# Kernel optimization log

Hardware: AMD Instinct MI355X
Metric: run time of the kernel (lower is better)

The kernel has to match this reference:

```python
import jax, jax.numpy as jnp
import numpy as np

H = 16       # num_heads (groups for complex conv)
A = 32       # num frequency anchors
KSZ = 5      # complex conv kernel size
PAD = (KSZ - 1) // 2  # circular padding, matches ComplexConv1DLayer


def setup_inputs() -> dict:
    key = jax.random.key(0)
    ks = jax.random.split(key, 12)
    B, N, D = 4, 2048, 1024
    hid, ghid = 256, 256  # pooling MLP hidden, gate MLP hidden
    F = N // 2 + 1

    def rn(k, shp, s=0.02):
        return jax.random.normal(k, shp, jnp.float32) * s

    return {
        "x": jax.random.normal(ks[0], (B, N, D), jnp.float32),
        "Wv": rn(ks[1], (D, D)), "bv": jnp.zeros((D,), jnp.float32),
        "Wp1": rn(ks[2], (D, hid)), "bp1": jnp.zeros((hid,), jnp.float32),
        "Wp2": rn(ks[3], (hid, 1)), "bp2": jnp.zeros((1,), jnp.float32),
        "Wg1": rn(ks[4], (D, ghid)), "bg1": jnp.zeros((ghid,), jnp.float32),
        "Wg2": rn(ks[5], (ghid, 2 * H * A)), "bg2": jnp.zeros((2 * H * A,), jnp.float32),
        "mod_bias": jnp.zeros((F,), jnp.float32),
        "conv_kr": rn(ks[6], (KSZ,), 1.0 / np.sqrt(KSZ)),
        "conv_ki": rn(ks[7], (KSZ,), 1.0 / np.sqrt(KSZ)),
        "Wo": rn(ks[8], (D, D)), "bo": jnp.zeros((D,), jnp.float32),
    }


def reference(x, Wv, bv, Wp1, bp1, Wp2, bp2, Wg1, bg1, Wg2, bg2,
              mod_bias, conv_kr, conv_ki, Wo, bo):
    B, N, D = x.shape
    dh = D // H
    F = N // 2 + 1

    # value projection -> per-head sequences, rFFT over sequence axis
    v = (x @ Wv + bv).reshape(B, N, H, dh).transpose(0, 2, 1, 3)   # (B,H,N,dh)
    Vf = jnp.fft.rfft(v, axis=2)                                   # (B,H,F,dh) complex64

    # AttentionPoolingLayer: two-layer MLP scores -> softmax over seq -> weighted sum
    s = jax.nn.gelu(x @ Wp1 + bp1, approximate=False) @ Wp2 + bp2  # (B,N,1)
    w = jax.nn.softmax(s, axis=1)
    g = jnp.sum(x * w, axis=1)                                     # (B,D)

    # gate MLP -> complex anchors (B,H,A)
    a = (jax.nn.gelu(g @ Wg1 + bg1, approximate=False) @ Wg2 + bg2).reshape(B, H, A, 2)
    anch_r, anch_i = a[..., 0], a[..., 1]

    # ComplexInterpolationLayer: cubic interpolation of anchors to F bins
    gr = jax.image.resize(anch_r, (B, H, F), method="cubic")
    gi = jax.image.resize(anch_i, (B, H, F), method="cubic")
    gate = gr + 1j * gi                                            # (B,H,F)

    # ComplexModReLULayer: ReLU(|z|+b) * z / |z| with per-frequency bias
    mag = jnp.abs(gate)
    gate = gate * (jax.nn.relu(mag + mod_bias) / (mag + 1e-8))

    # ComplexConv1DLayer: circular-pad complex conv along frequency
    gp = jnp.concatenate([gate[..., -PAD:], gate, gate[..., :PAD]], axis=-1)
    ker = conv_kr.astype(jnp.complex64) + 1j * conv_ki.astype(jnp.complex64)
    gate = sum(ker[j] * gp[..., j:j + F] for j in range(KSZ))      # (B,H,F)

    # spectral gating + inverse FFT + output projection
    y = jnp.fft.irfft(Vf * gate[..., None], n=N, axis=2)           # (B,H,N,dh)
    y = y.transpose(0, 2, 1, 3).reshape(B, N, D)
    return y @ Wo + bo
```

## Files before the change

### kernel.cpp

```cpp
#include <hip/hip_runtime.h>
#include <math.h>

#define NSEQ 2048
#define DMOD 1024
#define NBATCH 4
#define NHEAD 16
#define NFREQ 1025

typedef unsigned short u16t;
typedef __attribute__((ext_vector_type(8))) short short8;
typedef __attribute__((ext_vector_type(4))) float f32x4;

__device__ __forceinline__ float gelu_exact(float x) {
  return 0.5f * x * (1.0f + erff(x * 0.70710678118654752440f));
}
__device__ __forceinline__ u16t bf16_rtn(float x) {
  unsigned u = __float_as_uint(x);
  return (u16t)((u + 0x7FFFu + ((u >> 16) & 1u)) >> 16);
}
__device__ __forceinline__ float bf16f(u16t h) {
  return __uint_as_float(((unsigned)h) << 16);
}
__device__ __forceinline__ void gload_lds16(const u16t* g, u16t* l) {
  __builtin_amdgcn_global_load_lds(
      (const __attribute__((address_space(1))) void*)g,
      (__attribute__((address_space(3))) void*)l, 16, 0, 0);
}

__global__ __launch_bounds__(256) void split_kernel(const float* __restrict__ in,
    u16t* __restrict__ hi, u16t* __restrict__ lo, int n8) {
  for (int i = blockIdx.x * blockDim.x + threadIdx.x; i < n8; i += gridDim.x * blockDim.x) {
    const float4* p = reinterpret_cast<const float4*>(in + (size_t)i * 8);
    float4 a = p[0], b = p[1];
    float vv[8] = {a.x, a.y, a.z, a.w, b.x, b.y, b.z, b.w};
    alignas(16) u16t th[8];
    alignas(16) u16t tl[8];
#pragma unroll
    for (int e = 0; e < 8; ++e) {
      u16t h = bf16_rtn(vv[e]);
      th[e] = h;
      tl[e] = bf16_rtn(vv[e] - bf16f(h));
    }
    *reinterpret_cast<uint4*>(hi + (size_t)i * 8) = *reinterpret_cast<const uint4*>(th);
    *reinterpret_cast<uint4*>(lo + (size_t)i * 8) = *reinterpret_cast<const uint4*>(tl);
  }
}

__global__ __launch_bounds__(256) void tsplit_kernel(const float* __restrict__ W,
    u16t* __restrict__ Th, u16t* __restrict__ Tl, int K, int N) {
  __shared__ float tile[32][33];
  int k0 = blockIdx.y * 32, n0 = blockIdx.x * 32;
  int r = threadIdx.x >> 5, c = threadIdx.x & 31;
#pragma unroll
  for (int i = 0; i < 4; ++i)
    tile[r + 8 * i][c] = W[(size_t)(k0 + r + 8 * i) * N + n0 + c];
  __syncthreads();
#pragma unroll
  for (int i = 0; i < 4; ++i) {
    int rr = r + 8 * i;
    float v = tile[c][rr];
    u16t h = bf16_rtn(v);
    Th[(size_t)(n0 + rr) * K + k0 + c] = h;
    Tl[(size_t)(n0 + rr) * K + k0 + c] = bf16_rtn(v - bf16f(h));
  }
}

#define GEMM_KLOOP(Ah_g, Al_g, Bh_g, Bl_g, K, m0, n0)                                  \
  for (int k0 = 0; k0 < (K); k0 += 64) {                                               \
    _Pragma("unroll")                                                                  \
    for (int q = 0; q < 4; ++q) {                                                      \
      int cid = q * 256 + tid;                                                         \
      int row = cid >> 3, grp = cid & 7;                                               \
      int koff = k0 + ((grp ^ (row & 7)) << 3);                                        \
      size_t ea = (size_t)((m0) + row) * (K) + koff;                                   \
      size_t eb = (size_t)((n0) + row) * (K) + koff;                                   \
      int lbase = q * 2048 + wave * 512;                                               \
      gload_lds16((Ah_g) + ea, Ahs + lbase);                                           \
      gload_lds16((Al_g) + ea, Als + lbase);                                           \
      gload_lds16((Bh_g) + eb, Bhs + lbase);                                           \
      gload_lds16((Bl_g) + eb, Bls + lbase);                                           \
    }                                                                                  \
    __syncthreads();                                                                   \
    _Pragma("unroll")                                                                  \
    for (int kf = 0; kf < 2; ++kf) {                                                   \
      short8 ah[4], al[4];                                                             \
      _Pragma("unroll")                                                                \
      for (int mi = 0; mi < 4; ++mi) {                                                 \
        int r_ = wm0 + mi * 16 + lr;                                                   \
        int g = (kf * 4 + lg) ^ (r_ & 7);                                              \
        ah[mi] = *reinterpret_cast<const short8*>(&Ahs[r_ * 64 + g * 8]);              \
        al[mi] = *reinterpret_cast<const short8*>(&Als[r_ * 64 + g * 8]);              \
      }                                                                                \
      _Pragma("unroll")                                                                \
      for (int ni = 0; ni < 4; ++ni) {                                                 \
        int r_ = wn0 + ni * 16 + lr;                                                   \
        int g = (kf * 4 + lg) ^ (r_ & 7);                                              \
        short8 bh8 = *reinterpret_cast<const short8*>(&Bhs[r_ * 64 + g * 8]);          \
        short8 bl8 = *reinterpret_cast<const short8*>(&Bls[r_ * 64 + g * 8]);          \
        _Pragma("unroll")                                                              \
        for (int mi = 0; mi < 4; ++mi) {                                               \
          acc[mi][ni] = __builtin_amdgcn_mfma_f32_16x16x32_bf16(ah[mi], bh8, acc[mi][ni], 0, 0, 0); \
          acc[mi][ni] = __builtin_amdgcn_mfma_f32_16x16x32_bf16(ah[mi], bl8, acc[mi][ni], 0, 0, 0); \
          acc[mi][ni] = __builtin_amdgcn_mfma_f32_16x16x32_bf16(al[mi], bh8, acc[mi][ni], 0, 0, 0); \
        }                                                                              \
      }                                                                                \
    }                                                                                  \
    __syncthreads();                                                                   \
  }

__global__ __launch_bounds__(256) void gemm_fused_kernel(
    const u16t* __restrict__ Ah_g, const u16t* __restrict__ Al_g,
    const u16t* __restrict__ Bvh, const u16t* __restrict__ Bvl,
    const u16t* __restrict__ Bph, const u16t* __restrict__ Bpl,
    const float* __restrict__ bv, const float* __restrict__ bp1,
    const float* __restrict__ Wp2,
    float* __restrict__ vT, float* __restrict__ s_part) {
  __shared__ u16t Ahs[128 * 64], Als[128 * 64], Bhs[128 * 64], Bls[128 * 64];
  const int tid = threadIdx.x;
  const int lane = tid & 63, wave = tid >> 6;
  const int lr = lane & 15, lg = lane >> 4;
  const int wm0 = (wave >> 1) * 64, wn0 = (wave & 1) * 64;
  const int nwg = gridDim.x;
  const int L = (blockIdx.x & 7) * (nwg >> 3) + (blockIdx.x >> 3);
  const int m0 = (L / 10) * 128;
  const int nblk = L % 10;
  const bool vpath = (nblk < 8);
  const int n0 = vpath ? nblk * 128 : (nblk - 8) * 128;
  const u16t* Bh_g = vpath ? Bvh : Bph;
  const u16t* Bl_g = vpath ? Bvl : Bpl;
  const int K = 1024;

  f32x4 acc[4][4];
#pragma unroll
  for (int i = 0; i < 4; ++i)
#pragma unroll
    for (int j = 0; j < 4; ++j) acc[i][j] = 0.0f;

  GEMM_KLOOP(Ah_g, Al_g, Bh_g, Bl_g, K, m0, n0)

  if (vpath) {
#pragma unroll
    for (int mi = 0; mi < 4; ++mi)
#pragma unroll
      for (int ni = 0; ni < 4; ++ni) {
        int col = n0 + wn0 + ni * 16 + lr;
        float bvv = bv[col];
        f32x4 a = acc[mi][ni];
        int mbase = m0 + wm0 + mi * 16 + lg * 4;
        int b = mbase >> 11, ss = mbase & 2047;
        float4 o4;
        o4.x = a[0] + bvv; o4.y = a[1] + bvv; o4.z = a[2] + bvv; o4.w = a[3] + bvv;
        *reinterpret_cast<float4*>(vT + (size_t)b * (DMOD * NSEQ) + (size_t)col * NSEQ + ss) = o4;
      }
  } else {
    float w2[4], bcol[4];
#pragma unroll
    for (int ni = 0; ni < 4; ++ni) {
      int col = n0 + wn0 + ni * 16 + lr;
      w2[ni] = Wp2[col];
      bcol[ni] = bp1[col];
    }
    int chunk = (nblk - 8) * 2 + (wave & 1);
#pragma unroll
    for (int mi = 0; mi < 4; ++mi)
#pragma unroll
      for (int r = 0; r < 4; ++r) {
        float p = 0.f;
#pragma unroll
        for (int ni = 0; ni < 4; ++ni)
          p = fmaf(gelu_exact(acc[mi][ni][r] + bcol[ni]), w2[ni], p);
        p += __shfl_xor(p, 1);
        p += __shfl_xor(p, 2);
        p += __shfl_xor(p, 4);
        p += __shfl_xor(p, 8);
        if (lr == 0) {
          int row = m0 + wm0 + mi * 16 + lg * 4 + r;
          s_part[chunk * 8192 + row] = p;
        }
      }
  }
}

template<int NBLK>
__global__ __launch_bounds__(256) void mfma_gemm(
    const u16t* __restrict__ Ah_g, const u16t* __restrict__ Al_g,
    const u16t* __restrict__ Bh_g, const u16t* __restrict__ Bl_g,
    const float* __restrict__ bias,
    float* __restrict__ Cf,
    int N, int K) {
  __shared__ u16t Ahs[128 * 64], Als[128 * 64], Bhs[128 * 64], Bls[128 * 64];
  const int tid = threadIdx.x;
  const int lane = tid & 63, wave = tid >> 6;
  const int lr = lane & 15, lg = lane >> 4;
  const int wm0 = (wave >> 1) * 64, wn0 = (wave & 1) * 64;
  const int nwg = gridDim.x;
  const int L = (blockIdx.x & 7) * (nwg >> 3) + (blockIdx.x >> 3);
  const int m0 = (L / NBLK) * 128, n0 = (L % NBLK) * 128;

  f32x4 acc[4][4];
#pragma unroll
  for (int i = 0; i < 4; ++i)
#pragma unroll
    for (int j = 0; j < 4; ++j) acc[i][j] = 0.0f;

  GEMM_KLOOP(Ah_g, Al_g, Bh_g, Bl_g, K, m0, n0)

#pragma unroll
  for (int mi = 0; mi < 4; ++mi)
#pragma unroll
    for (int ni = 0; ni < 4; ++ni) {
      int col = n0 + wn0 + ni * 16 + lr;
      float bvv = bias[col];
      f32x4 a = acc[mi][ni];
#pragma unroll
      for (int r = 0; r < 4; ++r) {
        int row = m0 + wm0 + mi * 16 + lg * 4 + r;
        Cf[(size_t)row * N + col] = a[r] + bvv;
      }
    }
}

#define PADI(i) ((i) + ((i) >> 5))

template<int HJ, int TWS>
__device__ __forceinline__ void fwd_reg_stage(float* vr, float* vi,
    const float* TWr, const float* TWi, int lane) {
  float twr_[HJ], twi_[HJ];
#pragma unroll
  for (int t = 0; t < HJ; ++t) {
    int m = (t * 64 + lane) * TWS;
    twr_[t] = TWr[PADI(m)]; twi_[t] = TWi[PADI(m)];
  }
#pragma unroll
  for (int j = 0; j < 16; ++j) {
    if (j & HJ) continue;
    int t = j & (HJ - 1);
    float ur = vr[j], ui = vi[j];
    float wr = vr[j + HJ], wi = vi[j + HJ];
    float dr = ur - wr, di = ui - wi;
    vr[j] = ur + wr; vi[j] = ui + wi;
    vr[j + HJ] = dr * twr_[t] - di * twi_[t];
    vi[j + HJ] = dr * twi_[t] + di * twr_[t];
  }
}

template<int S, int TWS>
__device__ __forceinline__ void fwd_lane_stage(float* vr, float* vi,
    const float* TWr, const float* TWi, int lane) {
  float twr_ = 1.0f, twi_ = 0.0f;
  if (S > 1) {
    int m = (lane & (S - 1)) * TWS;
    twr_ = TWr[PADI(m)]; twi_ = TWi[PADI(m)];
  }
  bool hi = (lane & S) != 0;
#pragma unroll
  for (int j = 0; j < 16; ++j) {
    float or_ = __shfl_xor(vr[j], S, 64);
    float oi_ = __shfl_xor(vi[j], S, 64);
    float sr = vr[j] + or_, si_ = vi[j] + oi_;
    float dr = or_ - vr[j], di = oi_ - vi[j];
    float rr = dr * twr_ - di * twi_;
    float ri = dr * twi_ + di * twr_;
    vr[j] = hi ? rr : sr;
    vi[j] = hi ? ri : si_;
  }
}

template<int S, int TWS>
__device__ __forceinline__ void inv_lane_stage(float* vr, float* vi,
    const float* TWr, const float* TWi, int lane) {
  float twr_ = 1.0f, twi_ = 0.0f;
  if (S > 1) {
    int m = (lane & (S - 1)) * TWS;
    twr_ = TWr[PADI(m)]; twi_ = -TWi[PADI(m)];
  }
  bool hi = (lane & S) != 0;
#pragma unroll
  for (int j = 0; j < 16; ++j) {
    float xr = vr[j], xi = vi[j];
    if (S > 1) {
      float pr = xr * twr_ - xi * twi_;
      float pi = xr * twi_ + xi * twr_;
      xr = hi ? pr : xr;
      xi = hi ? pi : xi;
    }
    float or_ = __shfl_xor(xr, S, 64);
    float oi_ = __shfl_xor(xi, S, 64);
    vr[j] = hi ? (or_ - xr) : (xr + or_);
    vi[j] = hi ? (oi_ - xi) : (xi + oi_);
  }
}

template<int HJ, int TWS>
__device__ __forceinline__ void inv_reg_stage(float* vr, float* vi,
    const float* TWr, const float* TWi, int lane) {
  float twr_[HJ], twi_[HJ];
#pragma unroll
  for (int t = 0; t < HJ; ++t) {
    int m = (t * 64 + lane) * TWS;
    twr_[t] = TWr[PADI(m)]; twi_[t] = -TWi[PADI(m)];
  }
#pragma unroll
  for (int j = 0; j < 16; ++j) {
    if (j & HJ) continue;
    int t = j & (HJ - 1);
    float ur = vr[j], ui = vi[j];
    float br = vr[j + HJ], bi = vi[j + HJ];
    float wr = br * twr_[t] - bi * twi_[t];
    float wi = br * twi_[t] + bi * twr_[t];
    vr[j] = ur + wr; vi[j] = ui + wi;
    vr[j + HJ] = ur - wr; vi[j + HJ] = ui - wi;
  }
}

__global__ __launch_bounds__(256) void conv_fft_kernel(
    float* __restrict__ vio, const float* __restrict__ gateb) {
  __shared__ float Zr[4][1056], Zi[4][1056];
  __shared__ float TWr[528], TWi[528];
  const int tid = threadIdx.x;
  const int lane = tid & 63, wave = tid >> 6;
  const int c0 = blockIdx.x * 4;
  const int b = blockIdx.y;
  const int bh = b * NHEAD + (c0 >> 6);
  const float* gate_bh = gateb + (size_t)bh * NFREQ * 2;

#pragma unroll
  for (int q = 0; q < 2; ++q) {
    int m = q * 256 + tid;
    float si, co;
    sincosf(-3.14159265358979323846f * (float)m * (1.0f / 512.0f), &si, &co);
    TWr[PADI(m)] = co; TWi[PADI(m)] = si;
  }
  __syncthreads();

  float* zr = Zr[wave];
  float* zi = Zi[wave];
  float* col = vio + ((size_t)b * DMOD + (c0 + wave)) * NSEQ;

  float vr[16], vi[16];
#pragma unroll
  for (int j = 0; j < 16; ++j) {
    float2 w2 = *reinterpret_cast<const float2*>(col + 2 * (j * 64 + lane));
    vr[j] = w2.x; vi[j] = w2.y;
  }

  fwd_reg_stage<8, 1>(vr, vi, TWr, TWi, lane);
  fwd_reg_stage<4, 2>(vr, vi, TWr, TWi, lane);
  fwd_reg_stage<2, 4>(vr, vi, TWr, TWi, lane);
  fwd_reg_stage<1, 8>(vr, vi, TWr, TWi, lane);
  fwd_lane_stage<32, 16>(vr, vi, TWr, TWi, lane);
  fwd_lane_stage<16, 32>(vr, vi, TWr, TWi, lane);
  fwd_lane_stage<8, 64>(vr, vi, TWr, TWi, lane);
  fwd_lane_stage<4, 128>(vr, vi, TWr, TWi, lane);
  fwd_lane_stage<2, 256>(vr, vi, TWr, TWi, lane);
  fwd_lane_stage<1, 0>(vr, vi, TWr, TWi, lane);

#pragma unroll
  for (int j = 0; j < 16; ++j) {
    int p = PADI(j * 64 + lane);
    zr[p] = vr[j]; zi[p] = vi[j];
  }
  asm volatile("s_waitcnt lgkmcnt(0)" ::: "memory");

  const float s1 = 1.0f / 1024.0f;
#pragma unroll
  for (int q = 0; q < 8; ++q) {
    int k = q * 64 + lane;
    if (k == 0) {
      float z0r = zr[0], z0i = zi[0];
      float X0 = z0r + z0i;
      float XN = z0r - z0i;
      float2 G0 = *reinterpret_cast<const float2*>(gate_bh + 0);
      float2 GN = *reinterpret_cast<const float2*>(gate_bh + 1024 * 2);
      float y0 = X0 * G0.x * s1;
      float yN = XN * GN.x * s1;
      zr[0] = 0.5f * (y0 + yN); zi[0] = 0.5f * (y0 - yN);
      float zmr = zr[1], zmi = zi[1];
      float X5r = zmr, X5i = -zmi;
      float2 G5 = *reinterpret_cast<const float2*>(gate_bh + 512 * 2);
      float Y5r = (X5r * G5.x - X5i * G5.y) * s1;
      float Y5i = (X5r * G5.y + X5i * G5.x) * s1;
      zr[1] = Y5r; zi[1] = -Y5i;
    } else {
      int kq = 1024 - k;
      int rp = PADI((int)(__brev((unsigned)k) >> 22));
      int rq = PADI((int)(__brev((unsigned)kq) >> 22));
      float Zkr = zr[rp], Zki = zi[rp];
      float Zqr = zr[rq], Zqi = zi[rq];
      float Er = 0.5f * (Zkr + Zqr), Ei = 0.5f * (Zki - Zqi);
      float Odr = 0.5f * (Zki + Zqi), Odi = -0.5f * (Zkr - Zqr);
      float ti, tr;
      sincosf(-3.14159265358979323846f * (float)k * (1.0f / 1024.0f), &ti, &tr);
      float Pr = Odr * tr - Odi * ti, Pi = Odr * ti + Odi * tr;
      float Xkr = Er + Pr, Xki = Ei + Pi;
      float Xqr = Er - Pr, Xqi = -(Ei - Pi);
      float2 Gk = *reinterpret_cast<const float2*>(gate_bh + k * 2);
      float2 Gq = *reinterpret_cast<const float2*>(gate_bh + kq * 2);
      float Ykr = (Xkr * Gk.x - Xki * Gk.y) * s1;
      float Yki = (Xkr * Gk.y + Xki * Gk.x) * s1;
      float Yqr = (Xqr * Gq.x - Xqi * Gq.y) * s1;
      float Yqi = (Xqr * Gq.y + Xqi * Gq.x) * s1;
      float E2r = 0.5f * (Ykr + Yqr), E2i = 0.5f * (Yki - Yqi);
      float D2r = 0.5f * (Ykr - Yqr), D2i = 0.5f * (Yki + Yqi);
      float O2r = D2r * tr + D2i * ti, O2i = D2i * tr - D2r * ti;
      zr[rp] = E2r - O2i; zi[rp] = E2i + O2r;
      zr[rq] = E2r + O2i; zi[rq] = O2r - E2i;
    }
  }
  asm volatile("s_waitcnt lgkmcnt(0)" ::: "memory");

#pragma unroll
  for (int j = 0; j < 16; ++j) {
    int p = PADI(j * 64 + lane);
    vr[j] = zr[p]; vi[j] = zi[p];
  }
  asm volatile("s_waitcnt lgkmcnt(0)" ::: "memory");

  inv_lane_stage<1, 0>(vr, vi, TWr, TWi, lane);
  inv_lane_stage<2, 256>(vr, vi, TWr, TWi, lane);
  inv_lane_stage<4, 128>(vr, vi, TWr, TWi, lane);
  inv_lane_stage<8, 64>(vr, vi, TWr, TWi, lane);
  inv_lane_stage<16, 32>(vr, vi, TWr, TWi, lane);
  inv_lane_stage<32, 16>(vr, vi, TWr, TWi, lane);
  inv_reg_stage<1, 8>(vr, vi, TWr, TWi, lane);
  inv_reg_stage<2, 4>(vr, vi, TWr, TWi, lane);
  inv_reg_stage<4, 2>(vr, vi, TWr, TWi, lane);
  inv_reg_stage<8, 1>(vr, vi, TWr, TWi, lane);

#pragma unroll
  for (int j = 0; j < 16; ++j) {
    *reinterpret_cast<float2*>(col + 2 * (j * 64 + lane)) = make_float2(vr[j], vi[j]);
  }
}

__global__ __launch_bounds__(256) void tysplit_kernel(
    const float* __restrict__ yT, u16t* __restrict__ yh, u16t* __restrict__ yl) {
  __shared__ float tile[64][65];
  int t0 = blockIdx.x * 64, c0 = blockIdx.y * 64, b = blockIdx.z;
  int r = threadIdx.x >> 4;
  int cc = (threadIdx.x & 15) * 4;
#pragma unroll
  for (int i = 0; i < 4; ++i) {
    int row = r + 16 * i;
    float4 w = *reinterpret_cast<const float4*>(
        yT + ((size_t)b * DMOD + c0 + row) * NSEQ + t0 + cc);
    tile[row][cc] = w.x; tile[row][cc + 1] = w.y;
    tile[row][cc + 2] = w.z; tile[row][cc + 3] = w.w;
  }
  __syncthreads();
#pragma unroll
  for (int i = 0; i < 4; ++i) {
    int tt = r + 16 * i;
    alignas(8) u16t hh[4], ll[4];
#pragma unroll
    for (int e = 0; e < 4; ++e) {
      float v = tile[cc + e][tt];
      u16t h = bf16_rtn(v);
      hh[e] = h;
      ll[e] = bf16_rtn(v - bf16f(h));
    }
    size_t o = ((size_t)b * NSEQ + t0 + tt) * DMOD + c0 + cc;
    *reinterpret_cast<ushort4*>(yh + o) = *reinterpret_cast<const ushort4*>(hh);
    *reinterpret_cast<ushort4*>(yl + o) = *reinterpret_cast<const ushort4*>(ll);
  }
}

__global__ __launch_bounds__(256) void softmax_stats_kernel(
    const float* __restrict__ s_part, const float* __restrict__ bp2,
    float* __restrict__ s, float* __restrict__ bstats) {
  int b = blockIdx.x, tid = threadIdx.x;
  __shared__ float red[256];
  float bp = bp2[0];
  float m = -1e30f;
  for (int n = tid; n < NSEQ; n += 256) {
    int row = b * NSEQ + n;
    float v = s_part[row] + s_part[8192 + row] + s_part[2 * 8192 + row] +
              s_part[3 * 8192 + row] + bp;
    s[row] = v;
    m = fmaxf(m, v);
  }
  red[tid] = m; __syncthreads();
  for (int o = 128; o; o >>= 1) { if (tid < o) red[tid] = fmaxf(red[tid], red[tid + o]); __syncthreads(); }
  float bm = red[0]; __syncthreads();
  float sum = 0.f;
  for (int n = tid; n < NSEQ; n += 256) {
    int row = b * NSEQ + n;
    float v = s_part[row] + s_part[8192 + row] + s_part[2 * 8192 + row] +
              s_part[3 * 8192 + row] + bp;
    sum += expf(v - bm);
  }
  red[tid] = sum; __syncthreads();
  for (int o = 128; o; o >>= 1) { if (tid < o) red[tid] += red[tid + o]; __syncthreads(); }
  if (tid == 0) { bstats[b * 2] = bm; bstats[b * 2 + 1] = red[0]; }
}

__global__ __launch_bounds__(256) void pool_partial_kernel(
    const float* __restrict__ x, const float* __restrict__ s,
    const float* __restrict__ bstats, float* __restrict__ gpart) {
  int chunk = blockIdx.x, b = blockIdx.y;
  int tid = threadIdx.x;
  __shared__ float wsh[128];
  float bm = bstats[b * 2], inv = 1.0f / bstats[b * 2 + 1];
  int n0 = chunk * 128;
  if (tid < 128) wsh[tid] = expf(s[b * NSEQ + n0 + tid] - bm) * inv;
  __syncthreads();
  float acc[4] = {};
  for (int n = 0; n < 128; ++n) {
    float wn = wsh[n];
    const float* xr = &x[((size_t)b * NSEQ + n0 + n) * DMOD];
#pragma unroll
    for (int q = 0; q < 4; ++q) acc[q] = fmaf(wn, xr[tid + 256 * q], acc[q]);
  }
  float* gp = &gpart[((size_t)b * 16 + chunk) * DMOD];
#pragma unroll
  for (int q = 0; q < 4; ++q) gp[tid + 256 * q] = acc[q];
}

__global__ __launch_bounds__(256) void pool_reduce_mlp1_kernel(
    const float* __restrict__ gpart, const float* __restrict__ Wg1,
    float* __restrict__ part1) {
  int kb = blockIdx.x, b = blockIdx.y;
  int tid = threadIdx.x;
  int k0 = kb * 64;
  __shared__ float g_s[64];
  if (tid < 64) {
    float acc = 0.f;
#pragma unroll
    for (int j = 0; j < 16; ++j)
      acc += gpart[((size_t)b * 16 + j) * DMOD + k0 + tid];
    g_s[tid] = acc;
  }
  __syncthreads();
  float acc = 0.f;
#pragma unroll 8
  for (int i = 0; i < 64; ++i)
    acc = fmaf(g_s[i], Wg1[(size_t)(k0 + i) * 256 + tid], acc);
  part1[((size_t)b * 16 + kb) * 256 + tid] = acc;
}

__global__ __launch_bounds__(256) void mlp1red_mlp2_kernel(
    const float* __restrict__ part1, const float* __restrict__ bg1,
    const float* __restrict__ Wg2, float* __restrict__ part2) {
  int kb2 = blockIdx.x, nh = blockIdx.y, b = blockIdx.z;
  int tid = threadIdx.x;
  int k0 = kb2 * 64;
  __shared__ float hs_s[64];
  if (tid < 64) {
    float acc = bg1[k0 + tid];
#pragma unroll
    for (int j = 0; j < 16; ++j)
      acc += part1[((size_t)b * 16 + j) * 256 + k0 + tid];
    hs_s[tid] = gelu_exact(acc);
  }
  __syncthreads();
  float acc[2] = {};
#pragma unroll 8
  for (int i = 0; i < 64; ++i) {
    float hv = hs_s[i];
    const float* wr = &Wg2[(size_t)(k0 + i) * 1024 + nh * 512];
    acc[0] = fmaf(hv, wr[tid], acc[0]);
    acc[1] = fmaf(hv, wr[tid + 256], acc[1]);
  }
  float* pp = &part2[((size_t)b * 4 + kb2) * 1024 + nh * 512];
  pp[tid] = acc[0];
  pp[tid + 256] = acc[1];
}

__device__ __forceinline__ float keys_cubic(float x) {
  if (x >= 2.0f) return 0.0f;
  if (x >= 1.0f) return ((-0.5f * x + 2.5f) * x - 4.0f) * x + 2.0f;
  return ((1.5f * x - 2.5f) * x) * x + 1.0f;
}

__global__ __launch_bounds__(256) void gate_kernel(
    const float* __restrict__ part2, const float* __restrict__ bg2,
    const float* __restrict__ mod_bias,
    const float* __restrict__ kr5, const float* __restrict__ ki5,
    float* __restrict__ gate_out) {
  int bh = blockIdx.x;
  int tid = threadIdx.x;
  __shared__ float anch_s[64];
  __shared__ float ar_[32], ai_[32];
  __shared__ float gr[NFREQ], gi[NFREQ];
  int b = bh >> 4, h = bh & 15;
  if (tid < 64) {
    int cc = h * 64 + tid;
    float acc = bg2[cc];
#pragma unroll
    for (int j = 0; j < 4; ++j)
      acc += part2[((size_t)b * 4 + j) * 1024 + cc];
    anch_s[tid] = acc;
  }
  __syncthreads();
  if (tid < 32) {
    ar_[tid] = anch_s[tid * 2 + 0];
    ai_[tid] = anch_s[tid * 2 + 1];
  }
  __syncthreads();
  const float inv_scale = 32.0f / 1025.0f;
  for (int f = tid; f < NFREQ; f += 256) {
    float c = (f + 0.5f) * inv_scale - 0.5f;
    int j0 = (int)floorf(c) - 1;
    float wr = 0.f, wi = 0.f, wsum = 0.f;
#pragma unroll
    for (int u = 0; u < 4; ++u) {
      int j = j0 + u;
      if (j < 0 || j > 31) continue;
      float w = keys_cubic(fabsf(c - (float)j));
      wsum += w;
      wr = fmaf(w, ar_[j], wr);
      wi = fmaf(w, ai_[j], wi);
    }
    float invw = 1.0f / wsum;
    wr *= invw; wi *= invw;
    float mag = sqrtf(wr * wr + wi * wi);
    float scale = fmaxf(mag + mod_bias[f], 0.0f) / (mag + 1e-8f);
    gr[f] = wr * scale;
    gi[f] = wi * scale;
  }
  __syncthreads();
  float k_r[5], k_i[5];
#pragma unroll
  for (int j = 0; j < 5; ++j) { k_r[j] = kr5[j]; k_i[j] = ki5[j]; }
  for (int f = tid; f < NFREQ; f += 256) {
    float cr = 0.f, ci = 0.f;
#pragma unroll
    for (int j = 0; j < 5; ++j) {
      int idx = f + j - 2;
      if (idx < 0) idx += NFREQ;
      else if (idx >= NFREQ) idx -= NFREQ;
      float a = gr[idx], bb = gi[idx];
      cr = fmaf(k_r[j], a, cr); cr = fmaf(-k_i[j], bb, cr);
      ci = fmaf(k_r[j], bb, ci); ci = fmaf(k_i[j], a, ci);
    }
    gate_out[((size_t)bh * NFREQ + f) * 2 + 0] = cr;
    gate_out[((size_t)bh * NFREQ + f) * 2 + 1] = ci;
  }
}

extern "C" void kernel_launch(void* const* d_in, const int* in_sizes, int n_in,
                              void* d_out, int out_size, void* d_ws, size_t ws_size,
                              hipStream_t stream) {
  const float* x        = (const float*)d_in[0];
  const float* Wv       = (const float*)d_in[1];
  const float* bv       = (const float*)d_in[2];
  const float* Wp1      = (const float*)d_in[3];
  const float* bp1      = (const float*)d_in[4];
  const float* Wp2      = (const float*)d_in[5];
  const float* bp2      = (const float*)d_in[6];
  const float* Wg1      = (const float*)d_in[7];
  const float* bg1      = (const float*)d_in[8];
  const float* Wg2      = (const float*)d_in[9];
  const float* bg2      = (const float*)d_in[10];
  const float* mod_bias = (const float*)d_in[11];
  const float* ckr      = (const float*)d_in[12];
  const float* cki      = (const float*)d_in[13];
  const float* Wo       = (const float*)d_in[14];
  const float* bo       = (const float*)d_in[15];

  const int M = NBATCH * NSEQ;
  const size_t MD = (size_t)M * DMOD;
  char* wsb = (char*)d_ws;

  u16t* x_hi = (u16t*)wsb;
  u16t* x_lo = x_hi + MD;
  u16t* y_hi = x_hi;
  u16t* y_lo = x_lo;
  u16t* WT_h = (u16t*)(wsb + (size_t)32 * 1024 * 1024);
  u16t* WT_l = (u16t*)(wsb + (size_t)34 * 1024 * 1024);
  u16t* WTp1_h = (u16t*)(wsb + (size_t)36 * 1024 * 1024);
  u16t* WTp1_l = (u16t*)(wsb + (size_t)36 * 1024 * 1024 + 524288);
  float* s_part = (float*)(wsb + (size_t)37 * 1024 * 1024);
  float* s      = (float*)(wsb + (size_t)36 * 1024 * 1024);
  float* bstats = s + 8192;
  float* gpart  = bstats + 16;
  float* part1 = (float*)(wsb + (size_t)32 * 1024 * 1024);
  float* part2 = part1 + 4 * 16 * 256;
  float* gateb = (float*)(wsb + (size_t)32 * 1024 * 1024 + 65536);

  float* vT  = (float*)d_out;
  float* out = (float*)d_out;

  dim3 blk(256);

  split_kernel<<<dim3(2048), blk, 0, stream>>>(x, x_hi, x_lo, (int)(MD / 8));
  tsplit_kernel<<<dim3(1024 / 32, 1024 / 32), blk, 0, stream>>>(Wv, WT_h, WT_l, 1024, 1024);
  tsplit_kernel<<<dim3(256 / 32, 1024 / 32), blk, 0, stream>>>(Wp1, WTp1_h, WTp1_l, 1024, 256);
  gemm_fused_kernel<<<dim3(64 * 10), blk, 0, stream>>>(
      x_hi, x_lo, WT_h, WT_l, WTp1_h, WTp1_l, bv, bp1, Wp2, vT, s_part);
  softmax_stats_kernel<<<dim3(NBATCH), blk, 0, stream>>>(s_part, bp2, s, bstats);
  pool_partial_kernel<<<dim3(16, NBATCH), blk, 0, stream>>>(x, s, bstats, gpart);
  pool_reduce_mlp1_kernel<<<dim3(16, NBATCH), blk, 0, stream>>>(gpart, Wg1, part1);
  mlp1red_mlp2_kernel<<<dim3(4, 2, NBATCH), blk, 0, stream>>>(part1, bg1, Wg2, part2);
  gate_kernel<<<dim3(NBATCH * NHEAD), blk, 0, stream>>>(part2, bg2, mod_bias, ckr, cki, gateb);
  conv_fft_kernel<<<dim3(DMOD / 4, NBATCH), blk, 0, stream>>>(vT, gateb);
  tysplit_kernel<<<dim3(NSEQ / 64, DMOD / 64, NBATCH), blk, 0, stream>>>(vT, y_hi, y_lo);
  tsplit_kernel<<<dim3(1024 / 32, 1024 / 32), blk, 0, stream>>>(Wo, WT_h, WT_l, 1024, 1024);
  mfma_gemm<8><<<dim3((DMOD / 128) * (M / 128)), blk, 0, stream>>>(
      y_hi, y_lo, WT_h, WT_l, bo, out, DMOD, 1024);
}
```

Measured before the change: 228.6 us.

## Fold pooling-MLP GEMM slice into each value-projection block sharing the A tile

Before, the fused GEMM launched 640 blocks, 512 computing the value projection and 128 computing the pooling-MLP hidden layer, and each loaded the x tile separately. Now each of the 512 value blocks also computes a 32-column slice of the pooling MLP from the same LDS-resident x tile, so x is read once per block and the grid is a multiple of 256 CUs. The softmax stats kernel sums 8 partial score arrays instead of 4 and reuses the stored score in its second pass. The cost is extra LDS and registers per block, which may lower occupancy, and more MFMA work per block.

```diff
diff --git a/kernel.cpp b/kernel.cpp
--- a/kernel.cpp
+++ b/kernel.cpp
@@ -65,49 +65,6 @@
   }
 }
 
-#define GEMM_KLOOP(Ah_g, Al_g, Bh_g, Bl_g, K, m0, n0)                                  \
-  for (int k0 = 0; k0 < (K); k0 += 64) {                                               \
-    _Pragma("unroll")                                                                  \
-    for (int q = 0; q < 4; ++q) {                                                      \
-      int cid = q * 256 + tid;                                                         \
-      int row = cid >> 3, grp = cid & 7;                                               \
-      int koff = k0 + ((grp ^ (row & 7)) << 3);                                        \
-      size_t ea = (size_t)((m0) + row) * (K) + koff;                                   \
-      size_t eb = (size_t)((n0) + row) * (K) + koff;                                   \
-      int lbase = q * 2048 + wave * 512;                                               \
-      gload_lds16((Ah_g) + ea, Ahs + lbase);                                           \
-      gload_lds16((Al_g) + ea, Als + lbase);                                           \
-      gload_lds16((Bh_g) + eb, Bhs + lbase);                                           \
-      gload_lds16((Bl_g) + eb, Bls + lbase);                                           \
-    }                                                                                  \
-    __syncthreads();                                                                   \
-    _Pragma("unroll")                                                                  \
-    for (int kf = 0; kf < 2; ++kf) {                                                   \
-      short8 ah[4], al[4];                                                             \
-      _Pragma("unroll")                                                                \
-      for (int mi = 0; mi < 4; ++mi) {                                                 \
-        int r_ = wm0 + mi * 16 + lr;                                                   \
-        int g = (kf * 4 + lg) ^ (r_ & 7);                                              \
-        ah[mi] = *reinterpret_cast<const short8*>(&Ahs[r_ * 64 + g * 8]);              \
-        al[mi] = *reinterpret_cast<const short8*>(&Als[r_ * 64 + g * 8]);              \
-      }                                                                                \
-      _Pragma("unroll")                                                                \
-      for (int ni = 0; ni < 4; ++ni) {                                                 \
-        int r_ = wn0 + ni * 16 + lr;                                                   \
-        int g = (kf * 4 + lg) ^ (r_ & 7);                                              \
-        short8 bh8 = *reinterpret_cast<const short8*>(&Bhs[r_ * 64 + g * 8]);          \
-        short8 bl8 = *reinterpret_cast<const short8*>(&Bls[r_ * 64 + g * 8]);          \
-        _Pragma("unroll")                                                              \
-        for (int mi = 0; mi < 4; ++mi) {                                               \
-          acc[mi][ni] = __builtin_amdgcn_mfma_f32_16x16x32_bf16(ah[mi], bh8, acc[mi][ni], 0, 0, 0); \
-          acc[mi][ni] = __builtin_amdgcn_mfma_f32_16x16x32_bf16(ah[mi], bl8, acc[mi][ni], 0, 0, 0); \
-          acc[mi][ni] = __builtin_amdgcn_mfma_f32_16x16x32_bf16(al[mi], bh8, acc[mi][ni], 0, 0, 0); \
-        }                                                                              \
-      }                                                                                \
-    }                                                                                  \
-    __syncthreads();                                                                   \
-  }
-
 __global__ __launch_bounds__(256) void gemm_fused_kernel(
     const u16t* __restrict__ Ah_g, const u16t* __restrict__ Al_g,
     const u16t* __restrict__ Bvh, const u16t* __restrict__ Bvl,
@@ -116,18 +73,17 @@
     const float* __restrict__ Wp2,
     float* __restrict__ vT, float* __restrict__ s_part) {
   __shared__ u16t Ahs[128 * 64], Als[128 * 64], Bhs[128 * 64], Bls[128 * 64];
+  __shared__ u16t Php[32 * 64], Ppl[32 * 64];
   const int tid = threadIdx.x;
   const int lane = tid & 63, wave = tid >> 6;
   const int lr = lane & 15, lg = lane >> 4;
   const int wm0 = (wave >> 1) * 64, wn0 = (wave & 1) * 64;
   const int nwg = gridDim.x;
   const int L = (blockIdx.x & 7) * (nwg >> 3) + (blockIdx.x >> 3);
-  const int m0 = (L / 10) * 128;
-  const int nblk = L % 10;
-  const bool vpath = (nblk < 8);
-  const int n0 = vpath ? nblk * 128 : (nblk - 8) * 128;
-  const u16t* Bh_g = vpath ? Bvh : Bph;
-  const u16t* Bl_g = vpath ? Bvl : Bpl;
+  const int m0 = (L >> 3) * 128;
+  const int nblk = L & 7;
+  const int n0 = nblk * 128;
+  const int pc0 = nblk * 32;
   const int K = 1024;
 
   f32x4 acc[4][4];
@@ -135,47 +91,118 @@
   for (int i = 0; i < 4; ++i)
 #pragma unroll
     for (int j = 0; j < 4; ++j) acc[i][j] = 0.0f;
-
-  GEMM_KLOOP(Ah_g, Al_g, Bh_g, Bl_g, K, m0, n0)
-
-  if (vpath) {
-#pragma unroll
-    for (int mi = 0; mi < 4; ++mi)
+  f32x4 accp[2][2];
+#pragma unroll
+  for (int i = 0; i < 2; ++i)
+#pragma unroll
+    for (int j = 0; j < 2; ++j) accp[i][j] = 0.0f;
+
+  for (int k0 = 0; k0 < K; k0 += 64) {
+#pragma unroll
+    for (int q = 0; q < 4; ++q) {
+      int cid = q * 256 + tid;
+      int row = cid >> 3, grp = cid & 7;
+      int koff = k0 + ((grp ^ (row & 7)) << 3);
+      size_t ea = (size_t)(m0 + row) * K + koff;
+      size_t eb = (size_t)(n0 + row) * K + koff;
+      int lbase = q * 2048 + wave * 512;
+      gload_lds16(Ah_g + ea, Ahs + lbase);
+      gload_lds16(Al_g + ea, Als + lbase);
+      gload_lds16(Bvh + eb, Bhs + lbase);
+      gload_lds16(Bvl + eb, Bls + lbase);
+    }
+    {
+      int row = tid >> 3, grp = tid & 7;
+      int koff = k0 + ((grp ^ (row & 7)) << 3);
+      size_t ep = (size_t)(pc0 + row) * K + koff;
+      int lbase = wave * 512;
+      gload_lds16(Bph + ep, Php + lbase);
+      gload_lds16(Bpl + ep, Ppl + lbase);
+    }
+    __syncthreads();
+#pragma unroll
+    for (int kf = 0; kf < 2; ++kf) {
+      short8 ah[4], al[4];
+#pragma unroll
+      for (int mi = 0; mi < 4; ++mi) {
+        int r_ = wm0 + mi * 16 + lr;
+        int g = (kf * 4 + lg) ^ (r_ & 7);
+        ah[mi] = *reinterpret_cast<const short8*>(&Ahs[r_ * 64 + g * 8]);
+        al[mi] = *reinterpret_cast<const short8*>(&Als[r_ * 64 + g * 8]);
+      }
 #pragma unroll
       for (int ni = 0; ni < 4; ++ni) {
-        int col = n0 + wn0 + ni * 16 + lr;
-        float bvv = bv[col];
-        f32x4 a = acc[mi][ni];
-        int mbase = m0 + wm0 + mi * 16 + lg * 4;
-        int b = mbase >> 11, ss = mbase & 2047;
-        float4 o4;
-        o4.x = a[0] + bvv; o4.y = a[1] + bvv; o4.z = a[2] + bvv; o4.w = a[3] + bvv;
-        *reinterpret_cast<float4*>(vT + (size_t)b * (DMOD * NSEQ) + (size_t)col * NSEQ + ss) = o4;
+        int r_ = wn0 + ni * 16 + lr;
+        int g = (kf * 4 + lg) ^ (r_ & 7);
+        short8 bh8 = *reinterpret_cast<const short8*>(&Bhs[r_ * 64 + g * 8]);
+        short8 bl8 = *reinterpret_cast<const short8*>(&Bls[r_ * 64 + g * 8]);
+#pragma unroll
+        for (int mi = 0; mi < 4; ++mi) {
+          acc[mi][ni] = __builtin_amdgcn_mfma_f32_16x16x32_bf16(ah[mi], bh8, acc[mi][ni], 0, 0, 0);
+          acc[mi][ni] = __builtin_amdgcn_mfma_f32_16x16x32_bf16(ah[mi], bl8, acc[mi][ni], 0, 0, 0);
+          acc[mi][ni] = __builtin_amdgcn_mfma_f32_16x16x32_bf16(al[mi], bh8, acc[mi][ni], 0, 0, 0);
+        }
       }
-  } else {
-    float w2[4], bcol[4];
+      short8 pah[2], pal[2];
+#pragma unroll
+      for (int mi = 0; mi < 2; ++mi) {
+        int r_ = wave * 32 + mi * 16 + lr;
+        int g = (kf * 4 + lg) ^ (r_ & 7);
+        pah[mi] = *reinterpret_cast<const short8*>(&Ahs[r_ * 64 + g * 8]);
+        pal[mi] = *reinterpret_cast<const short8*>(&Als[r_ * 64 + g * 8]);
+      }
+#pragma unroll
+      for (int ni = 0; ni < 2; ++ni) {
+        int r_ = ni * 16 + lr;
+        int g = (kf * 4 + lg) ^ (r_ & 7);
+        short8 pbh = *reinterpret_cast<const short8*>(&Php[r_ * 64 + g * 8]);
+        short8 pbl = *reinterpret_cast<const short8*>(&Ppl[r_ * 64 + g * 8]);
+#pragma unroll
+        for (int mi = 0; mi < 2; ++mi) {
+          accp[mi][ni] = __builtin_amdgcn_mfma_f32_16x16x32_bf16(pah[mi], pbh, accp[mi][ni], 0, 0, 0);
+          accp[mi][ni] = __builtin_amdgcn_mfma_f32_16x16x32_bf16(pah[mi], pbl, accp[mi][ni], 0, 0, 0);
+          accp[mi][ni] = __builtin_amdgcn_mfma_f32_16x16x32_bf16(pal[mi], pbh, accp[mi][ni], 0, 0, 0);
+        }
+      }
+    }
+    __syncthreads();
+  }
+#pragma unroll
+  for (int mi = 0; mi < 4; ++mi)
 #pragma unroll
     for (int ni = 0; ni < 4; ++ni) {
       int col = n0 + wn0 + ni * 16 + lr;
+      float bvv = bv[col];
+      f32x4 a = acc[mi][ni];
+      int mbase = m0 + wm0 + mi * 16 + lg * 4;
+      int b = mbase >> 11, ss = mbase & 2047;
+      float4 o4;
+      o4.x = a[0] + bvv; o4.y = a[1] + bvv; o4.z = a[2] + bvv; o4.w = a[3] + bvv;
+      *reinterpret_cast<float4*>(vT + (size_t)b * (DMOD * NSEQ) + (size_t)col * NSEQ + ss) = o4;
+    }
+  {
+    float w2[2], bcol[2];
+#pragma unroll
+    for (int ni = 0; ni < 2; ++ni) {
+      int col = pc0 + ni * 16 + lr;
       w2[ni] = Wp2[col];
       bcol[ni] = bp1[col];
     }
-    int chunk = (nblk - 8) * 2 + (wave & 1);
-#pragma unroll
-    for (int mi = 0; mi < 4; ++mi)
+#pragma unroll
+    for (int mi = 0; mi < 2; ++mi)
 #pragma unroll
       for (int r = 0; r < 4; ++r) {
         float p = 0.f;
 #pragma unroll
-        for (int ni = 0; ni < 4; ++ni)
-          p = fmaf(gelu_exact(acc[mi][ni][r] + bcol[ni]), w2[ni], p);
+        for (int ni = 0; ni < 2; ++ni)
+          p = fmaf(gelu_exact(accp[mi][ni][r] + bcol[ni]), w2[ni], p);
         p += __shfl_xor(p, 1);
         p += __shfl_xor(p, 2);
         p += __shfl_xor(p, 4);
         p += __shfl_xor(p, 8);
         if (lr == 0) {
-          int row = m0 + wm0 + mi * 16 + lg * 4 + r;
-          s_part[chunk * 8192 + row] = p;
+          int row = m0 + wave * 32 + mi * 16 + lg * 4 + r;
+          s_part[nblk * 8192 + row] = p;
         }
       }
   }
@@ -203,8 +230,47 @@
 #pragma unroll
     for (int j = 0; j < 4; ++j) acc[i][j] = 0.0f;
 
-  GEMM_KLOOP(Ah_g, Al_g, Bh_g, Bl_g, K, m0, n0)
-
+  for (int k0 = 0; k0 < K; k0 += 64) {
+#pragma unroll
+    for (int q = 0; q < 4; ++q) {
+      int cid = q * 256 + tid;
+      int row = cid >> 3, grp = cid & 7;
+      int koff = k0 + ((grp ^ (row & 7)) << 3);
+      size_t ea = (size_t)(m0 + row) * K + koff;
+      size_t eb = (size_t)(n0 + row) * K + koff;
+      int lbase = q * 2048 + wave * 512;
+      gload_lds16(Ah_g + ea, Ahs + lbase);
+      gload_lds16(Al_g + ea, Als + lbase);
+      gload_lds16(Bh_g + eb, Bhs + lbase);
+      gload_lds16(Bl_g + eb, Bls + lbase);
+    }
+    __syncthreads();
+#pragma unroll
+    for (int kf = 0; kf < 2; ++kf) {
+      short8 ah[4], al[4];
+#pragma unroll
+      for (int mi = 0; mi < 4; ++mi) {
+        int r_ = wm0 + mi * 16 + lr;
+        int g = (kf * 4 + lg) ^ (r_ & 7);
+        ah[mi] = *reinterpret_cast<const short8*>(&Ahs[r_ * 64 + g * 8]);
+        al[mi] = *reinterpret_cast<const short8*>(&Als[r_ * 64 + g * 8]);
+      }
+#pragma unroll
+      for (int ni = 0; ni < 4; ++ni) {
+        int r_ = wn0 + ni * 16 + lr;
+        int g = (kf * 4 + lg) ^ (r_ & 7);
+        short8 bh8 = *reinterpret_cast<const short8*>(&Bhs[r_ * 64 + g * 8]);
+        short8 bl8 = *reinterpret_cast<const short8*>(&Bls[r_ * 64 + g * 8]);
+#pragma unroll
+        for (int mi = 0; mi < 4; ++mi) {
+          acc[mi][ni] = __builtin_amdgcn_mfma_f32_16x16x32_bf16(ah[mi], bh8, acc[mi][ni], 0, 0, 0);
+          acc[mi][ni] = __builtin_amdgcn_mfma_f32_16x16x32_bf16(ah[mi], bl8, acc[mi][ni], 0, 0, 0);
+          acc[mi][ni] = __builtin_amdgcn_mfma_f32_16x16x32_bf16(al[mi], bh8, acc[mi][ni], 0, 0, 0);
+        }
+      }
+    }
+    __syncthreads();
+  }
 #pragma unroll
   for (int mi = 0; mi < 4; ++mi)
 #pragma unroll
@@ -474,8 +540,9 @@
   float m = -1e30f;
   for (int n = tid; n < NSEQ; n += 256) {
     int row = b * NSEQ + n;
-    float v = s_part[row] + s_part[8192 + row] + s_part[2 * 8192 + row] +
-              s_part[3 * 8192 + row] + bp;
+    float v = bp;
+#pragma unroll
+    for (int c = 0; c < 8; ++c) v += s_part[c * 8192 + row];
     s[row] = v;
     m = fmaxf(m, v);
   }
@@ -483,12 +550,7 @@
   for (int o = 128; o; o >>= 1) { if (tid < o) red[tid] = fmaxf(red[tid], red[tid + o]); __syncthreads(); }
   float bm = red[0]; __syncthreads();
   float sum = 0.f;
-  for (int n = tid; n < NSEQ; n += 256) {
-    int row = b * NSEQ + n;
-    float v = s_part[row] + s_part[8192 + row] + s_part[2 * 8192 + row] +
-              s_part[3 * 8192 + row] + bp;
-    sum += expf(v - bm);
-  }
+  for (int n = tid; n < NSEQ; n += 256) sum += expf(s[b * NSEQ + n] - bm);
   red[tid] = sum; __syncthreads();
   for (int o = 128; o; o >>= 1) { if (tid < o) red[tid] += red[tid + o]; __syncthreads(); }
   if (tid == 0) { bstats[b * 2] = bm; bstats[b * 2 + 1] = red[0]; }
@@ -686,7 +748,7 @@
   split_kernel<<<dim3(2048), blk, 0, stream>>>(x, x_hi, x_lo, (int)(MD / 8));
   tsplit_kernel<<<dim3(1024 / 32, 1024 / 32), blk, 0, stream>>>(Wv, WT_h, WT_l, 1024, 1024);
   tsplit_kernel<<<dim3(256 / 32, 1024 / 32), blk, 0, stream>>>(Wp1, WTp1_h, WTp1_l, 1024, 256);
-  gemm_fused_kernel<<<dim3(64 * 10), blk, 0, stream>>>(
+  gemm_fused_kernel<<<dim3(512), blk, 0, stream>>>(
       x_hi, x_lo, WT_h, WT_l, WTp1_h, WTp1_l, bv, bp1, Wp2, vT, s_part);
   softmax_stats_kernel<<<dim3(NBATCH), blk, 0, stream>>>(s_part, bp2, s, bstats);
   pool_partial_kernel<<<dim3(16, NBATCH), blk, 0, stream>>>(x, s, bstats, gpart);
```

Measured after the change: 206.0 us. 1.11x faster.
